# Optimization experiments

Hardware: AMD Instinct MI355X
Metric: run time of the kernel (lower is better)

The kernel has to match this reference:

```python
import jax, jax.numpy as jnp
import numpy as np

RES = 128            # occupancy grid resolution per axis
HIDDEN = 128         # MLP width
PE_POS = 10          # positional-encoding freqs for xyz
PE_DIR = 4           # positional-encoding freqs for viewdirs
S_MAX = 192          # max marching steps per ray
STEP = 0.027         # render_step_size (~aabb diagonal / S_MAX)
ERT = 1e-4           # early_stop_eps (transmittance threshold)
AABB_MIN = -1.5
AABB_MAX = 1.5
WHITE_BKGD = 1.0     # white_bkgd=True


def _posenc(x, L):
    # x: [..., 3] -> [..., 3 + 6L]
    freqs = 2.0 ** jnp.arange(L, dtype=x.dtype)
    xb = x[..., None, :] * freqs[:, None]                 # [..., L, 3]
    enc = jnp.concatenate([jnp.sin(xb), jnp.cos(xb)], axis=-1)  # [..., L, 6]
    return jnp.concatenate([x, enc.reshape(x.shape[:-1] + (-1,))], axis=-1)


def setup_inputs() -> dict:
    key = jax.random.key(0)
    ks = jax.random.split(key, 8)
    B, N = 1, 2048
    # camera origins on a sphere of radius 2.5 outside the aabb, rays aimed near the center
    o = jax.random.normal(ks[0], (B, N, 3), dtype=jnp.float32)
    o = o / jnp.linalg.norm(o, axis=-1, keepdims=True) * 2.5
    target = jax.random.normal(ks[1], (B, N, 3), dtype=jnp.float32) * 0.3
    d = target - o
    d = d / jnp.linalg.norm(d, axis=-1, keepdims=True)
    occ_grid = jax.random.bernoulli(ks[2], 0.3, (RES, RES, RES))
    din_pos = 3 + 6 * PE_POS   # 63
    din_dir = 3 + 6 * PE_DIR   # 27
    sc = lambda n: 1.0 / np.sqrt(n)
    W0 = jax.random.normal(ks[3], (din_pos, HIDDEN), dtype=jnp.float32) * sc(din_pos)
    W1 = jax.random.normal(ks[4], (HIDDEN, HIDDEN), dtype=jnp.float32) * sc(HIDDEN)
    w_sigma = jax.random.normal(ks[5], (HIDDEN, 1), dtype=jnp.float32) * sc(HIDDEN)
    W2 = jax.random.normal(ks[6], (HIDDEN + din_dir, HIDDEN), dtype=jnp.float32) * sc(HIDDEN)
    w_rgb = jax.random.normal(ks[7], (HIDDEN, 3), dtype=jnp.float32) * sc(HIDDEN)
    return {"rays_o": o, "viewdirs": d, "occ_grid": occ_grid,
            "W0": W0, "W1": W1, "w_sigma": w_sigma, "W2": W2, "w_rgb": w_rgb}


def reference(rays_o, viewdirs, occ_grid, W0, W1, w_sigma, W2, w_rgb):
    B, N, _ = rays_o.shape
    o = rays_o.reshape(-1, 3)          # [R, 3]
    d = viewdirs.reshape(-1, 3)        # [R, 3]
    R = o.shape[0]
    # ray / aabb intersection
    inv_d = 1.0 / jnp.where(jnp.abs(d) < 1e-9, 1e-9, d)
    t0 = (AABB_MIN - o) * inv_d
    t1 = (AABB_MAX - o) * inv_d
    t_near = jnp.maximum(jnp.max(jnp.minimum(t0, t1), axis=-1), 0.0)  # [R]
    t_far = jnp.min(jnp.maximum(t0, t1), axis=-1)                     # [R]
    # fixed-step marching (padded to S_MAX, masked) == nerfacc sampling with occ grid
    i = jnp.arange(S_MAX, dtype=rays_o.dtype)
    t_start = t_near[:, None] + STEP * i[None, :]   # [R, S]
    t_end = t_start + STEP
    t_mid = t_start + 0.5 * STEP
    inside = (t_mid < t_far[:, None]) & ((t_far > t_near)[:, None])
    pts = o[:, None, :] + d[:, None, :] * t_mid[..., None]  # [R, S, 3]
    # occupancy lookup (skip empty cells)
    gidx = jnp.clip(((pts - AABB_MIN) / (AABB_MAX - AABB_MIN) * RES).astype(jnp.int32), 0, RES - 1)
    occ = occ_grid[gidx[..., 0], gidx[..., 1], gidx[..., 2]]  # [R, S] bool
    mask = inside & occ
    # NeRF MLP (rgb_alpha_fn): sigma from pos, rgb from pos feature + viewdir
    pe_p = _posenc(pts.reshape(-1, 3), PE_POS)                               # [RS, 63]
    pe_d = _posenc(jnp.broadcast_to(d[:, None, :], pts.shape).reshape(-1, 3), PE_DIR)  # [RS, 27]
    h = jax.nn.relu(pe_p @ W0)
    h = jax.nn.relu(h @ W1)
    sigma = (h @ w_sigma).reshape(R, S_MAX)
    h2 = jax.nn.relu(jnp.concatenate([h, pe_d], axis=-1) @ W2)
    rgb = jax.nn.sigmoid(h2 @ w_rgb).reshape(R, S_MAX, 3)
    # alpha compositing (nerfacc.rendering) with early termination
    delta = t_end - t_start
    alpha = (1.0 - jnp.exp(-jax.nn.relu(sigma) * delta)) * mask.astype(sigma.dtype)
    trans = jnp.cumprod(1.0 - alpha + 1e-10, axis=-1)
    T = jnp.concatenate([jnp.ones((R, 1), alpha.dtype), trans[:, :-1]], axis=-1)  # exclusive
    T = T * (T > ERT).astype(T.dtype)  # early ray termination
    w = T * alpha                      # [R, S]
    rgb_map = jnp.einsum('rs,rsc->rc', w, rgb)
    opacity = jnp.sum(w, axis=-1, keepdims=True)
    depth = jnp.sum(w * t_mid, axis=-1, keepdims=True)
    rgb_map = rgb_map + (1.0 - opacity) * WHITE_BKGD
    return (rgb_map.reshape(B, N, 3), depth.reshape(B, N, 1), opacity.reshape(B, N, 1))
```

## Files before the change

### kernel.cpp

```cpp
#include <hip/hip_runtime.h>
#include <stdint.h>

#define NRAYS 2048
#define SMAX  192
#define RESG  128
#define STEPF 0.027f
#define ERTF  1e-4f

typedef __attribute__((ext_vector_type(8)))  short bf16x8;
typedef __attribute__((ext_vector_type(16))) float f32x16;

__device__ __forceinline__ uint32_t f2b(float x) {
    uint32_t u = __builtin_bit_cast(uint32_t, x);
    return (u + 0x7fffu + ((u >> 16) & 1u)) >> 16;
}
__device__ __forceinline__ uint32_t bpack(float lo, float hi) {
    return f2b(lo) | (f2b(hi) << 16);
}

__device__ __forceinline__ void ray_aabb(float ox, float oy, float oz,
                                         float dx, float dy, float dz,
                                         float& tn, float& tf) {
    float ix = 1.0f / ((fabsf(dx) < 1e-9f) ? 1e-9f : dx);
    float iy = 1.0f / ((fabsf(dy) < 1e-9f) ? 1e-9f : dy);
    float iz = 1.0f / ((fabsf(dz) < 1e-9f) ? 1e-9f : dz);
    float t0x = (-1.5f - ox) * ix, t1x = (1.5f - ox) * ix;
    float t0y = (-1.5f - oy) * iy, t1y = (1.5f - oy) * iy;
    float t0z = (-1.5f - oz) * iz, t1z = (1.5f - oz) * iz;
    float tnx = fminf(t0x, t1x), tfx = fmaxf(t0x, t1x);
    float tny = fminf(t0y, t1y), tfy = fmaxf(t0y, t1y);
    float tnz = fminf(t0z, t1z), tfz = fmaxf(t0z, t1z);
    tn = fmaxf(fmaxf(fmaxf(tnx, tny), tnz), 0.0f);
    tf = fminf(fminf(tfx, tfy), tfz);
}

__global__ __launch_bounds__(512) void k_fused(
        const float* __restrict__ ro, const float* __restrict__ rd,
        const int* __restrict__ occ,
        const float* __restrict__ W0, const float* __restrict__ W1,
        const float* __restrict__ wsig, const float* __restrict__ W2,
        const float* __restrict__ wrgb, float* __restrict__ out) {
    __shared__ __align__(16) short actA[128 * 128];
    __shared__ __align__(16) short bufB[128 * 256];
    __shared__ float4 rgbaL[8 * SMAX];
    __shared__ unsigned short sList[8 * SMAX];
    __shared__ float  sPD[8][28];
    __shared__ float  sRD[8][8];
    __shared__ float  sV[128];
    __shared__ float  sR[384];
    __shared__ int    sCnt[8];

    const int tid  = threadIdx.x;
    const int wave = tid >> 6;
    const int lane = tid & 63;
    const int oc   = wave & 3;
    const int sc   = wave >> 2;
    const int lo5  = lane & 31;
    const int hi5  = lane >> 5;

    if (tid < 128) sV[tid] = wsig[tid];
    if (tid >= 128 && tid < 512) sR[tid - 128] = wrgb[tid - 128];

    bf16x8 wf[22];
    {
        const int outc = oc * 32 + lo5;
        #pragma unroll
        for (int g = 0; g < 22; ++g) {
            const float* W; int kbase, Klim;
            if (g < 4)       { W = W0; kbase = g * 16;        Klim = 63;  }
            else if (g < 12) { W = W1; kbase = (g - 4) * 16;  Klim = 128; }
            else             { W = W2; kbase = (g - 12) * 16; Klim = 155; }
            uint32_t d[4];
            #pragma unroll
            for (int h = 0; h < 4; ++h) {
                int k0 = kbase + (hi5 << 3) + h * 2;
                float lo = (k0     < Klim) ? W[(size_t)k0 * 128 + outc]       : 0.0f;
                float hi = (k0 + 1 < Klim) ? W[(size_t)(k0 + 1) * 128 + outc] : 0.0f;
                d[h] = bpack(lo, hi);
            }
            uint4 v = make_uint4(d[0], d[1], d[2], d[3]);
            wf[g] = __builtin_bit_cast(bf16x8, v);
        }
    }

    const int r = blockIdx.x * 8 + wave;
    const float ox = ro[r*3+0], oy = ro[r*3+1], oz = ro[r*3+2];
    const float dx = rd[r*3+0], dy = rd[r*3+1], dz = rd[r*3+2];
    float tn, tf;
    ray_aabb(ox, oy, oz, dx, dy, dz, tn, tf);
    unsigned long long msk[3];
    int myCnt = 0;
    #pragma unroll
    for (int c = 0; c < 3; ++c) {
        int s = c * 64 + lane;
        float t_mid = (tn + STEPF * (float)s) + 0.5f * STEPF;
        bool inside = (t_mid < tf) && (tf > tn);
        bool act = false;
        if (inside) {
            float px = ox + dx * t_mid;
            float py = oy + dy * t_mid;
            float pz = oz + dz * t_mid;
            int gx = min(max((int)((px + 1.5f) / 3.0f * 128.0f), 0), RESG - 1);
            int gy = min(max((int)((py + 1.5f) / 3.0f * 128.0f), 0), RESG - 1);
            int gz = min(max((int)((pz + 1.5f) / 3.0f * 128.0f), 0), RESG - 1);
            act = occ[(gx * RESG + gy) * RESG + gz] != 0;
        }
        unsigned long long mb = __ballot(act);
        msk[c] = mb;
        myCnt += __popcll(mb);
    }
    if (lane == 0) {
        sCnt[wave] = myCnt;
        sRD[wave][0] = ox; sRD[wave][1] = oy; sRD[wave][2] = oz;
        sRD[wave][3] = dx; sRD[wave][4] = dy; sRD[wave][5] = dz;
        sRD[wave][6] = tn;
    }
    if (lane < 28) {
        float val = 0.0f;
        if (lane < 3) val = (lane == 0) ? dx : ((lane == 1) ? dy : dz);
        else if (lane < 27) {
            int cc = lane - 3, l = cc / 6, jj = cc - 6 * l;
            int a3 = (jj >= 3) ? jj - 3 : jj;
            float comp = (a3 == 0) ? dx : ((a3 == 1) ? dy : dz);
            float arg = comp * (float)(1 << l);
            val = (jj < 3) ? __sinf(arg) : __cosf(arg);
        }
        sPD[wave][lane] = val;
    }
    __syncthreads();

    int myBase = 0, total = 0;
    #pragma unroll
    for (int i = 0; i < 8; ++i) {
        int ci = sCnt[i];
        if (i < wave) myBase += ci;
        total += ci;
    }
    {
        int run = myBase;
        #pragma unroll
        for (int c = 0; c < 3; ++c) {
            unsigned long long mb = msk[c];
            if ((mb >> lane) & 1ull) {
                int within = __popcll(mb & ((1ull << lane) - 1ull));
                sList[run + within] = (unsigned short)((wave << 8) | (c * 64 + lane));
            }
            run += __popcll(mb);
        }
    }
    __syncthreads();

    const int ntiles = (total + 127) >> 7;
    const int mrow   = sc * 64 + lo5;
    const int rswz   = (mrow & 15) << 4;

    for (int t = 0; t < ntiles; ++t) {
        const int base = t << 7;
        __syncthreads();

        {
            int m = tid >> 2, p = tid & 3;
            int gi = base + m;
            float px = 0.f, py = 0.f, pz = 0.f;
            int we = 0;
            if (gi < total) {
                int e = sList[gi];
                we = e >> 8;
                int s = e & 255;
                float tnw = sRD[we][6];
                float t_mid = (tnw + STEPF * (float)s) + 0.5f * STEPF;
                px = sRD[we][0] + sRD[we][3] * t_mid;
                py = sRD[we][1] + sRD[we][4] * t_mid;
                pz = sRD[we][2] + sRD[we][5] * t_mid;
            }
            int swz = (m & 15) << 4;
            #pragma unroll
            for (int half = 0; half < 2; ++half) {
                uint32_t dw[4];
                #pragma unroll
                for (int jp = 0; jp < 4; ++jp) {
                    float v[2];
                    #pragma unroll
                    for (int q = 0; q < 2; ++q) {
                        int c = p * 16 + half * 8 + jp * 2 + q;
                        float val;
                        if (c < 3)        val = (c == 0) ? px : ((c == 1) ? py : pz);
                        else if (c >= 63) val = 0.0f;
                        else {
                            int cc = c - 3, l = cc / 6, jj = cc - 6 * l;
                            int a3 = (jj >= 3) ? jj - 3 : jj;
                            float comp = (a3 == 0) ? px : ((a3 == 1) ? py : pz);
                            float arg = comp * (float)(1 << l);
                            val = (jj < 3) ? __sinf(arg) : __cosf(arg);
                        }
                        v[q] = val;
                    }
                    dw[jp] = bpack(v[0], v[1]);
                }
                *(uint4*)((char*)actA + m * 256 + ((p * 32 + half * 16) ^ swz)) = make_uint4(dw[0], dw[1], dw[2], dw[3]);
            }
            {
                uint32_t dw[4];
                #pragma unroll
                for (int jp = 0; jp < 4; ++jp) {
                    float v[2];
                    #pragma unroll
                    for (int q = 0; q < 2; ++q) {
                        int c = p * 8 + jp * 2 + q;
                        v[q] = (c < 28) ? sPD[we][c] : 0.0f;
                    }
                    dw[jp] = bpack(v[0], v[1]);
                }
                *(uint4*)((char*)bufB + m * 512 + ((256 + p * 16) ^ swz)) = make_uint4(dw[0], dw[1], dw[2], dw[3]);
            }
        }
        __syncthreads();

        {
            f32x16 a0 = {}, a1 = {};
            #pragma unroll
            for (int kb = 0; kb < 4; ++kb) {
                int cb = (kb * 32 + (hi5 << 4)) ^ rswz;
                bf16x8 b0 = *(const bf16x8*)((const char*)actA + mrow * 256 + cb);
                bf16x8 b1 = *(const bf16x8*)((const char*)actA + (mrow + 32) * 256 + cb);
                a0 = __builtin_amdgcn_mfma_f32_32x32x16_bf16(wf[kb], b0, a0, 0, 0, 0);
                a1 = __builtin_amdgcn_mfma_f32_32x32x16_bf16(wf[kb], b1, a1, 0, 0, 0);
            }
            #pragma unroll
            for (int g = 0; g < 4; ++g) {
                int outb = (oc * 32 + g * 8 + (hi5 << 2)) * 2;
                *(uint2*)((char*)bufB + mrow * 512 + (outb ^ rswz)) =
                    make_uint2(bpack(fmaxf(a0[g*4+0],0.f), fmaxf(a0[g*4+1],0.f)),
                               bpack(fmaxf(a0[g*4+2],0.f), fmaxf(a0[g*4+3],0.f)));
                *(uint2*)((char*)bufB + (mrow + 32) * 512 + (outb ^ rswz)) =
                    make_uint2(bpack(fmaxf(a1[g*4+0],0.f), fmaxf(a1[g*4+1],0.f)),
                               bpack(fmaxf(a1[g*4+2],0.f), fmaxf(a1[g*4+3],0.f)));
            }
        }
        __syncthreads();

        {
            f32x16 a0 = {}, a1 = {};
            #pragma unroll
            for (int kb = 0; kb < 8; ++kb) {
                int cb = (kb * 32 + (hi5 << 4)) ^ rswz;
                bf16x8 b0 = *(const bf16x8*)((const char*)bufB + mrow * 512 + cb);
                bf16x8 b1 = *(const bf16x8*)((const char*)bufB + (mrow + 32) * 512 + cb);
                a0 = __builtin_amdgcn_mfma_f32_32x32x16_bf16(wf[4 + kb], b0, a0, 0, 0, 0);
                a1 = __builtin_amdgcn_mfma_f32_32x32x16_bf16(wf[4 + kb], b1, a1, 0, 0, 0);
            }
            #pragma unroll
            for (int g = 0; g < 4; ++g) {
                int outb = (oc * 32 + g * 8 + (hi5 << 2)) * 2;
                *(uint2*)((char*)actA + mrow * 256 + (outb ^ rswz)) =
                    make_uint2(bpack(fmaxf(a0[g*4+0],0.f), fmaxf(a0[g*4+1],0.f)),
                               bpack(fmaxf(a0[g*4+2],0.f), fmaxf(a0[g*4+3],0.f)));
                *(uint2*)((char*)actA + (mrow + 32) * 256 + (outb ^ rswz)) =
                    make_uint2(bpack(fmaxf(a1[g*4+0],0.f), fmaxf(a1[g*4+1],0.f)),
                               bpack(fmaxf(a1[g*4+2],0.f), fmaxf(a1[g*4+3],0.f)));
            }
        }
        __syncthreads();

        {
            f32x16 a0 = {}, a1 = {};
            #pragma unroll
            for (int kb = 0; kb < 8; ++kb) {
                int cb = (kb * 32 + (hi5 << 4)) ^ rswz;
                bf16x8 b0 = *(const bf16x8*)((const char*)actA + mrow * 256 + cb);
                bf16x8 b1 = *(const bf16x8*)((const char*)actA + (mrow + 32) * 256 + cb);
                a0 = __builtin_amdgcn_mfma_f32_32x32x16_bf16(wf[12 + kb], b0, a0, 0, 0, 0);
                a1 = __builtin_amdgcn_mfma_f32_32x32x16_bf16(wf[12 + kb], b1, a1, 0, 0, 0);
            }
            #pragma unroll
            for (int kb = 8; kb < 10; ++kb) {
                int cb = (kb * 32 + (hi5 << 4)) ^ rswz;
                bf16x8 b0 = *(const bf16x8*)((const char*)bufB + mrow * 512 + cb);
                bf16x8 b1 = *(const bf16x8*)((const char*)bufB + (mrow + 32) * 512 + cb);
                a0 = __builtin_amdgcn_mfma_f32_32x32x16_bf16(wf[12 + kb], b0, a0, 0, 0, 0);
                a1 = __builtin_amdgcn_mfma_f32_32x32x16_bf16(wf[12 + kb], b1, a1, 0, 0, 0);
            }
            #pragma unroll
            for (int g = 0; g < 4; ++g) {
                int outb = (oc * 32 + g * 8 + (hi5 << 2)) * 2;
                *(uint2*)((char*)bufB + mrow * 512 + (outb ^ rswz)) =
                    make_uint2(bpack(fmaxf(a0[g*4+0],0.f), fmaxf(a0[g*4+1],0.f)),
                               bpack(fmaxf(a0[g*4+2],0.f), fmaxf(a0[g*4+3],0.f)));
                *(uint2*)((char*)bufB + (mrow + 32) * 512 + (outb ^ rswz)) =
                    make_uint2(bpack(fmaxf(a1[g*4+0],0.f), fmaxf(a1[g*4+1],0.f)),
                               bpack(fmaxf(a1[g*4+2],0.f), fmaxf(a1[g*4+3],0.f)));
            }
        }
        __syncthreads();

        {
            int m = tid >> 2, p = tid & 3;
            int gi = base + m;
            int swz = (m & 15) << 4;
            float sp = 0.f, r0 = 0.f, r1 = 0.f, r2 = 0.f;
            #pragma unroll
            for (int hh = 0; hh < 4; ++hh) {
                uint4 q = *(const uint4*)((const char*)actA + m * 256 + ((p * 64 + hh * 16) ^ swz));
                uint32_t w[4] = {q.x, q.y, q.z, q.w};
                #pragma unroll
                for (int e = 0; e < 4; ++e) {
                    int j = p * 32 + hh * 8 + e * 2;
                    float a0 = __builtin_bit_cast(float, w[e] << 16);
                    float a1 = __builtin_bit_cast(float, w[e] & 0xffff0000u);
                    sp = fmaf(a0, sV[j], sp);
                    sp = fmaf(a1, sV[j + 1], sp);
                }
            }
            #pragma unroll
            for (int hh = 0; hh < 4; ++hh) {
                uint4 q = *(const uint4*)((const char*)bufB + m * 512 + ((p * 64 + hh * 16) ^ swz));
                uint32_t w[4] = {q.x, q.y, q.z, q.w};
                #pragma unroll
                for (int e = 0; e < 4; ++e) {
                    int j = p * 32 + hh * 8 + e * 2;
                    float a0 = __builtin_bit_cast(float, w[e] << 16);
                    float a1 = __builtin_bit_cast(float, w[e] & 0xffff0000u);
                    r0 = fmaf(a0, sR[j*3+0], r0); r1 = fmaf(a0, sR[j*3+1], r1); r2 = fmaf(a0, sR[j*3+2], r2);
                    r0 = fmaf(a1, sR[(j+1)*3+0], r0); r1 = fmaf(a1, sR[(j+1)*3+1], r1); r2 = fmaf(a1, sR[(j+1)*3+2], r2);
                }
            }
            #pragma unroll
            for (int off = 1; off < 4; off <<= 1) {
                sp += __shfl_xor(sp, off);
                r0 += __shfl_xor(r0, off);
                r1 += __shfl_xor(r1, off);
                r2 += __shfl_xor(r2, off);
            }
            if (p == 0 && gi < total) {
                float alpha = 1.0f - __expf(-fmaxf(sp, 0.0f) * STEPF);
                float c0 = 1.0f / (1.0f + __expf(-r0));
                float c1 = 1.0f / (1.0f + __expf(-r1));
                float c2 = 1.0f / (1.0f + __expf(-r2));
                rgbaL[gi] = make_float4(c0, c1, c2, alpha);
            }
        }
    }
    __syncthreads();

    {
        float T_run = 1.0f;
        float cr = 0.f, cg = 0.f, cb = 0.f, opa = 0.f, dep = 0.f;
        for (int j = 0; j < myCnt; j += 64) {
            int idx = j + lane;
            float4 f = make_float4(0.f, 0.f, 0.f, 0.f);
            float tmid = 0.f;
            if (idx < myCnt) {
                f = rgbaL[myBase + idx];
                int s = sList[myBase + idx] & 255;
                tmid = (tn + STEPF * (float)s) + 0.5f * STEPF;
            }
            float p = (1.0f - f.w) + 1e-10f;
            #pragma unroll
            for (int o = 1; o < 64; o <<= 1) {
                float v = __shfl_up(p, o);
                if (lane >= o) p *= v;
            }
            float pprev = __shfl_up(p, 1);
            float Texc = (lane == 0) ? T_run : T_run * pprev;
            Texc = (Texc > ERTF) ? Texc : 0.0f;
            float w = Texc * f.w;
            cr += w * f.x; cg += w * f.y; cb += w * f.z;
            opa += w; dep += w * tmid;
            T_run *= __shfl(p, 63);
            if (T_run <= ERTF) break;
        }
        #pragma unroll
        for (int o = 32; o; o >>= 1) {
            cr  += __shfl_xor(cr, o);
            cg  += __shfl_xor(cg, o);
            cb  += __shfl_xor(cb, o);
            opa += __shfl_xor(opa, o);
            dep += __shfl_xor(dep, o);
        }
        if (lane == 0) {
            out[r * 3 + 0] = cr + (1.0f - opa);
            out[r * 3 + 1] = cg + (1.0f - opa);
            out[r * 3 + 2] = cb + (1.0f - opa);
            out[NRAYS * 3 + r] = dep;
            out[NRAYS * 4 + r] = opa;
        }
    }
}

extern "C" void kernel_launch(void* const* d_in, const int* in_sizes, int n_in,
                              void* d_out, int out_size, void* d_ws, size_t ws_size,
                              hipStream_t stream) {
    const float* ro   = (const float*)d_in[0];
    const float* rd   = (const float*)d_in[1];
    const int*   occ  = (const int*)d_in[2];
    const float* W0   = (const float*)d_in[3];
    const float* W1   = (const float*)d_in[4];
    const float* wsig = (const float*)d_in[5];
    const float* W2   = (const float*)d_in[6];
    const float* wrgb = (const float*)d_in[7];
    float* out = (float*)d_out;

    k_fused<<<NRAYS / 8, 512, 0, stream>>>(ro, rd, occ, W0, W1, wsig, W2, wrgb, out);
}
```

Before: 115.6 us.

## Halve rays per block to four and use 64-row MLP tiles

Each 512-thread block now handles 4 rays instead of 8, doubling the grid to 512 blocks. The MLP tile shrinks from 128 to 64 sample rows, so each wave runs one MFMA chain instead of two. Encoding and head work is split across 8 threads per row. Shared memory drops to about half, and launch bounds request 4 blocks per CU, to raise occupancy and spread work over more CUs on a small problem. The cost is that half the waves sit idle during ray setup and compositing, per-block weight fragment loads double in total, and per-tile sync overhead becomes relatively larger.

After: 189.7 us. 1.64x slower.

```diff
diff --git a/kernel.cpp b/kernel.cpp
--- a/kernel.cpp
+++ b/kernel.cpp
@@ -34,21 +34,21 @@
     tf = fminf(fminf(tfx, tfy), tfz);
 }
 
-__global__ __launch_bounds__(512) void k_fused(
+__global__ __launch_bounds__(512, 4) void k_fused(
         const float* __restrict__ ro, const float* __restrict__ rd,
         const int* __restrict__ occ,
         const float* __restrict__ W0, const float* __restrict__ W1,
         const float* __restrict__ wsig, const float* __restrict__ W2,
         const float* __restrict__ wrgb, float* __restrict__ out) {
-    __shared__ __align__(16) short actA[128 * 128];
-    __shared__ __align__(16) short bufB[128 * 256];
-    __shared__ float4 rgbaL[8 * SMAX];
-    __shared__ unsigned short sList[8 * SMAX];
-    __shared__ float  sPD[8][28];
-    __shared__ float  sRD[8][8];
+    __shared__ __align__(16) short actA[64 * 128];
+    __shared__ __align__(16) short bufB[64 * 256];
+    __shared__ float4 rgbaL[4 * SMAX];
+    __shared__ unsigned short sList[4 * SMAX];
+    __shared__ float  sPD[4][28];
+    __shared__ float  sRD[4][8];
     __shared__ float  sV[128];
     __shared__ float  sR[384];
-    __shared__ int    sCnt[8];
+    __shared__ int    sCnt[4];
 
     const int tid  = threadIdx.x;
     const int wave = tid >> 6;
@@ -83,60 +83,63 @@
         }
     }
 
-    const int r = blockIdx.x * 8 + wave;
-    const float ox = ro[r*3+0], oy = ro[r*3+1], oz = ro[r*3+2];
-    const float dx = rd[r*3+0], dy = rd[r*3+1], dz = rd[r*3+2];
-    float tn, tf;
-    ray_aabb(ox, oy, oz, dx, dy, dz, tn, tf);
     unsigned long long msk[3];
     int myCnt = 0;
-    #pragma unroll
-    for (int c = 0; c < 3; ++c) {
-        int s = c * 64 + lane;
-        float t_mid = (tn + STEPF * (float)s) + 0.5f * STEPF;
-        bool inside = (t_mid < tf) && (tf > tn);
-        bool act = false;
-        if (inside) {
-            float px = ox + dx * t_mid;
-            float py = oy + dy * t_mid;
-            float pz = oz + dz * t_mid;
-            int gx = min(max((int)((px + 1.5f) / 3.0f * 128.0f), 0), RESG - 1);
-            int gy = min(max((int)((py + 1.5f) / 3.0f * 128.0f), 0), RESG - 1);
-            int gz = min(max((int)((pz + 1.5f) / 3.0f * 128.0f), 0), RESG - 1);
-            act = occ[(gx * RESG + gy) * RESG + gz] != 0;
-        }
-        unsigned long long mb = __ballot(act);
-        msk[c] = mb;
-        myCnt += __popcll(mb);
-    }
-    if (lane == 0) {
-        sCnt[wave] = myCnt;
-        sRD[wave][0] = ox; sRD[wave][1] = oy; sRD[wave][2] = oz;
-        sRD[wave][3] = dx; sRD[wave][4] = dy; sRD[wave][5] = dz;
-        sRD[wave][6] = tn;
-    }
-    if (lane < 28) {
-        float val = 0.0f;
-        if (lane < 3) val = (lane == 0) ? dx : ((lane == 1) ? dy : dz);
-        else if (lane < 27) {
-            int cc = lane - 3, l = cc / 6, jj = cc - 6 * l;
-            int a3 = (jj >= 3) ? jj - 3 : jj;
-            float comp = (a3 == 0) ? dx : ((a3 == 1) ? dy : dz);
-            float arg = comp * (float)(1 << l);
-            val = (jj < 3) ? __sinf(arg) : __cosf(arg);
-        }
-        sPD[wave][lane] = val;
+    float tn = 0.f;
+    const int r = blockIdx.x * 4 + wave;
+    if (wave < 4) {
+        const float ox = ro[r*3+0], oy = ro[r*3+1], oz = ro[r*3+2];
+        const float dx = rd[r*3+0], dy = rd[r*3+1], dz = rd[r*3+2];
+        float tf;
+        ray_aabb(ox, oy, oz, dx, dy, dz, tn, tf);
+        #pragma unroll
+        for (int c = 0; c < 3; ++c) {
+            int s = c * 64 + lane;
+            float t_mid = (tn + STEPF * (float)s) + 0.5f * STEPF;
+            bool inside = (t_mid < tf) && (tf > tn);
+            bool act = false;
+            if (inside) {
+                float px = ox + dx * t_mid;
+                float py = oy + dy * t_mid;
+                float pz = oz + dz * t_mid;
+                int gx = min(max((int)((px + 1.5f) / 3.0f * 128.0f), 0), RESG - 1);
+                int gy = min(max((int)((py + 1.5f) / 3.0f * 128.0f), 0), RESG - 1);
+                int gz = min(max((int)((pz + 1.5f) / 3.0f * 128.0f), 0), RESG - 1);
+                act = occ[(gx * RESG + gy) * RESG + gz] != 0;
+            }
+            unsigned long long mb = __ballot(act);
+            msk[c] = mb;
+            myCnt += __popcll(mb);
+        }
+        if (lane == 0) {
+            sCnt[wave] = myCnt;
+            sRD[wave][0] = ox; sRD[wave][1] = oy; sRD[wave][2] = oz;
+            sRD[wave][3] = dx; sRD[wave][4] = dy; sRD[wave][5] = dz;
+            sRD[wave][6] = tn;
+        }
+        if (lane < 28) {
+            float val = 0.0f;
+            if (lane < 3) val = (lane == 0) ? dx : ((lane == 1) ? dy : dz);
+            else if (lane < 27) {
+                int cc = lane - 3, l = cc / 6, jj = cc - 6 * l;
+                int a3 = (jj >= 3) ? jj - 3 : jj;
+                float comp = (a3 == 0) ? dx : ((a3 == 1) ? dy : dz);
+                float arg = comp * (float)(1 << l);
+                val = (jj < 3) ? __sinf(arg) : __cosf(arg);
+            }
+            sPD[wave][lane] = val;
+        }
     }
     __syncthreads();
 
     int myBase = 0, total = 0;
     #pragma unroll
-    for (int i = 0; i < 8; ++i) {
+    for (int i = 0; i < 4; ++i) {
         int ci = sCnt[i];
         if (i < wave) myBase += ci;
         total += ci;
     }
-    {
+    if (wave < 4) {
         int run = myBase;
         #pragma unroll
         for (int c = 0; c < 3; ++c) {
@@ -150,16 +153,16 @@
     }
     __syncthreads();
 
-    const int ntiles = (total + 127) >> 7;
-    const int mrow   = sc * 64 + lo5;
+    const int ntiles = (total + 63) >> 6;
+    const int mrow   = sc * 32 + lo5;
     const int rswz   = (mrow & 15) << 4;
 
     for (int t = 0; t < ntiles; ++t) {
-        const int base = t << 7;
-        __syncthreads();
-
-        {
-            int m = tid >> 2, p = tid & 3;
+        const int base = t << 6;
+        __syncthreads();
+
+        {
+            int m = tid >> 3, p = tid & 7;
             int gi = base + m;
             float px = 0.f, py = 0.f, pz = 0.f;
             int we = 0;
@@ -174,33 +177,29 @@
                 pz = sRD[we][2] + sRD[we][5] * t_mid;
             }
             int swz = (m & 15) << 4;
-            #pragma unroll
-            for (int half = 0; half < 2; ++half) {
-                uint32_t dw[4];
+            uint32_t dw[4];
+            #pragma unroll
+            for (int jp = 0; jp < 4; ++jp) {
+                float v[2];
                 #pragma unroll
-                for (int jp = 0; jp < 4; ++jp) {
-                    float v[2];
-                    #pragma unroll
-                    for (int q = 0; q < 2; ++q) {
-                        int c = p * 16 + half * 8 + jp * 2 + q;
-                        float val;
-                        if (c < 3)        val = (c == 0) ? px : ((c == 1) ? py : pz);
-                        else if (c >= 63) val = 0.0f;
-                        else {
-                            int cc = c - 3, l = cc / 6, jj = cc - 6 * l;
-                            int a3 = (jj >= 3) ? jj - 3 : jj;
-                            float comp = (a3 == 0) ? px : ((a3 == 1) ? py : pz);
-                            float arg = comp * (float)(1 << l);
-                            val = (jj < 3) ? __sinf(arg) : __cosf(arg);
-                        }
-                        v[q] = val;
+                for (int q = 0; q < 2; ++q) {
+                    int c = p * 8 + jp * 2 + q;
+                    float val;
+                    if (c < 3)        val = (c == 0) ? px : ((c == 1) ? py : pz);
+                    else if (c >= 63) val = 0.0f;
+                    else {
+                        int cc = c - 3, l = cc / 6, jj = cc - 6 * l;
+                        int a3 = (jj >= 3) ? jj - 3 : jj;
+                        float comp = (a3 == 0) ? px : ((a3 == 1) ? py : pz);
+                        float arg = comp * (float)(1 << l);
+                        val = (jj < 3) ? __sinf(arg) : __cosf(arg);
                     }
-                    dw[jp] = bpack(v[0], v[1]);
+                    v[q] = val;
                 }
-                *(uint4*)((char*)actA + m * 256 + ((p * 32 + half * 16) ^ swz)) = make_uint4(dw[0], dw[1], dw[2], dw[3]);
-            }
-            {
-                uint32_t dw[4];
+                dw[jp] = bpack(v[0], v[1]);
+            }
+            *(uint4*)((char*)actA + m * 256 + ((p * 16) ^ swz)) = make_uint4(dw[0], dw[1], dw[2], dw[3]);
+            if (p < 4) {
                 #pragma unroll
                 for (int jp = 0; jp < 4; ++jp) {
                     float v[2];
@@ -217,94 +216,73 @@
         __syncthreads();
 
         {
-            f32x16 a0 = {}, a1 = {};
+            f32x16 acc = {};
             #pragma unroll
             for (int kb = 0; kb < 4; ++kb) {
-                int cb = (kb * 32 + (hi5 << 4)) ^ rswz;
-                bf16x8 b0 = *(const bf16x8*)((const char*)actA + mrow * 256 + cb);
-                bf16x8 b1 = *(const bf16x8*)((const char*)actA + (mrow + 32) * 256 + cb);
-                a0 = __builtin_amdgcn_mfma_f32_32x32x16_bf16(wf[kb], b0, a0, 0, 0, 0);
-                a1 = __builtin_amdgcn_mfma_f32_32x32x16_bf16(wf[kb], b1, a1, 0, 0, 0);
+                bf16x8 bf = *(const bf16x8*)((const char*)actA + mrow * 256 + ((kb * 32 + (hi5 << 4)) ^ rswz));
+                acc = __builtin_amdgcn_mfma_f32_32x32x16_bf16(wf[kb], bf, acc, 0, 0, 0);
             }
             #pragma unroll
             for (int g = 0; g < 4; ++g) {
                 int outb = (oc * 32 + g * 8 + (hi5 << 2)) * 2;
                 *(uint2*)((char*)bufB + mrow * 512 + (outb ^ rswz)) =
-                    make_uint2(bpack(fmaxf(a0[g*4+0],0.f), fmaxf(a0[g*4+1],0.f)),
-                               bpack(fmaxf(a0[g*4+2],0.f), fmaxf(a0[g*4+3],0.f)));
-                *(uint2*)((char*)bufB + (mrow + 32) * 512 + (outb ^ rswz)) =
-                    make_uint2(bpack(fmaxf(a1[g*4+0],0.f), fmaxf(a1[g*4+1],0.f)),
-                               bpack(fmaxf(a1[g*4+2],0.f), fmaxf(a1[g*4+3],0.f)));
-            }
-        }
-        __syncthreads();
-
-        {
-            f32x16 a0 = {}, a1 = {};
+                    make_uint2(bpack(fmaxf(acc[g*4+0],0.f), fmaxf(acc[g*4+1],0.f)),
+                               bpack(fmaxf(acc[g*4+2],0.f), fmaxf(acc[g*4+3],0.f)));
+            }
+        }
+        __syncthreads();
+
+        {
+            f32x16 acc = {};
             #pragma unroll
             for (int kb = 0; kb < 8; ++kb) {
-                int cb = (kb * 32 + (hi5 << 4)) ^ rswz;
-                bf16x8 b0 = *(const bf16x8*)((const char*)bufB + mrow * 512 + cb);
-                bf16x8 b1 = *(const bf16x8*)((const char*)bufB + (mrow + 32) * 512 + cb);
-                a0 = __builtin_amdgcn_mfma_f32_32x32x16_bf16(wf[4 + kb], b0, a0, 0, 0, 0);
-                a1 = __builtin_amdgcn_mfma_f32_32x32x16_bf16(wf[4 + kb], b1, a1, 0, 0, 0);
+                bf16x8 bf = *(const bf16x8*)((const char*)bufB + mrow * 512 + ((kb * 32 + (hi5 << 4)) ^ rswz));
+                acc = __builtin_amdgcn_mfma_f32_32x32x16_bf16(wf[4 + kb], bf, acc, 0, 0, 0);
             }
             #pragma unroll
             for (int g = 0; g < 4; ++g) {
                 int outb = (oc * 32 + g * 8 + (hi5 << 2)) * 2;
                 *(uint2*)((char*)actA + mrow * 256 + (outb ^ rswz)) =
-                    make_uint2(bpack(fmaxf(a0[g*4+0],0.f), fmaxf(a0[g*4+1],0.f)),
-                               bpack(fmaxf(a0[g*4+2],0.f), fmaxf(a0[g*4+3],0.f)));
-                *(uint2*)((char*)actA + (mrow + 32) * 256 + (outb ^ rswz)) =
-                    make_uint2(bpack(fmaxf(a1[g*4+0],0.f), fmaxf(a1[g*4+1],0.f)),
-                               bpack(fmaxf(a1[g*4+2],0.f), fmaxf(a1[g*4+3],0.f)));
-            }
-        }
-        __syncthreads();
-
-        {
-            f32x16 a0 = {}, a1 = {};
+                    make_uint2(bpack(fmaxf(acc[g*4+0],0.f), fmaxf(acc[g*4+1],0.f)),
+                               bpack(fmaxf(acc[g*4+2],0.f), fmaxf(acc[g*4+3],0.f)));
+            }
+        }
+        __syncthreads();
+
+        {
+            f32x16 acc = {};
             #pragma unroll
             for (int kb = 0; kb < 8; ++kb) {
-                int cb = (kb * 32 + (hi5 << 4)) ^ rswz;
-                bf16x8 b0 = *(const bf16x8*)((const char*)actA + mrow * 256 + cb);
-                bf16x8 b1 = *(const bf16x8*)((const char*)actA + (mrow + 32) * 256 + cb);
-                a0 = __builtin_amdgcn_mfma_f32_32x32x16_bf16(wf[12 + kb], b0, a0, 0, 0, 0);
-                a1 = __builtin_amdgcn_mfma_f32_32x32x16_bf16(wf[12 + kb], b1, a1, 0, 0, 0);
+                bf16x8 bf = *(const bf16x8*)((const char*)actA + mrow * 256 + ((kb * 32 + (hi5 << 4)) ^ rswz));
+                acc = __builtin_amdgcn_mfma_f32_32x32x16_bf16(wf[12 + kb], bf, acc, 0, 0, 0);
             }
             #pragma unroll
             for (int kb = 8; kb < 10; ++kb) {
-                int cb = (kb * 32 + (hi5 << 4)) ^ rswz;
-                bf16x8 b0 = *(const bf16x8*)((const char*)bufB + mrow * 512 + cb);
-                bf16x8 b1 = *(const bf16x8*)((const char*)bufB + (mrow + 32) * 512 + cb);
-                a0 = __builtin_amdgcn_mfma_f32_32x32x16_bf16(wf[12 + kb], b0, a0, 0, 0, 0);
-                a1 = __builtin_amdgcn_mfma_f32_32x32x16_bf16(wf[12 + kb], b1, a1, 0, 0, 0);
+                bf16x8 bf = *(const bf16x8*)((const char*)bufB + mrow * 512 + ((kb * 32 + (hi5 << 4)) ^ rswz));
+                acc = __builtin_amdgcn_mfma_f32_32x32x16_bf16(wf[12 + kb], bf, acc, 0, 0, 0);
             }
             #pragma unroll
             for (int g = 0; g < 4; ++g) {
                 int outb = (oc * 32 + g * 8 + (hi5 << 2)) * 2;
                 *(uint2*)((char*)bufB + mrow * 512 + (outb ^ rswz)) =
-                    make_uint2(bpack(fmaxf(a0[g*4+0],0.f), fmaxf(a0[g*4+1],0.f)),
-                               bpack(fmaxf(a0[g*4+2],0.f), fmaxf(a0[g*4+3],0.f)));
-                *(uint2*)((char*)bufB + (mrow + 32) * 512 + (outb ^ rswz)) =
-                    make_uint2(bpack(fmaxf(a1[g*4+0],0.f), fmaxf(a1[g*4+1],0.f)),
-                               bpack(fmaxf(a1[g*4+2],0.f), fmaxf(a1[g*4+3],0.f)));
-            }
-        }
-        __syncthreads();
-
-        {
-            int m = tid >> 2, p = tid & 3;
+                    make_uint2(bpack(fmaxf(acc[g*4+0],0.f), fmaxf(acc[g*4+1],0.f)),
+                               bpack(fmaxf(acc[g*4+2],0.f), fmaxf(acc[g*4+3],0.f)));
+            }
+        }
+        __syncthreads();
+
+        {
+            int m = tid >> 3, p = tid & 7;
             int gi = base + m;
             int swz = (m & 15) << 4;
             float sp = 0.f, r0 = 0.f, r1 = 0.f, r2 = 0.f;
             #pragma unroll
-            for (int hh = 0; hh < 4; ++hh) {
-                uint4 q = *(const uint4*)((const char*)actA + m * 256 + ((p * 64 + hh * 16) ^ swz));
+            for (int hh = 0; hh < 2; ++hh) {
+                uint4 q = *(const uint4*)((const char*)actA + m * 256 + ((p * 32 + hh * 16) ^ swz));
                 uint32_t w[4] = {q.x, q.y, q.z, q.w};
                 #pragma unroll
                 for (int e = 0; e < 4; ++e) {
-                    int j = p * 32 + hh * 8 + e * 2;
+                    int j = p * 16 + hh * 8 + e * 2;
                     float a0 = __builtin_bit_cast(float, w[e] << 16);
                     float a1 = __builtin_bit_cast(float, w[e] & 0xffff0000u);
                     sp = fmaf(a0, sV[j], sp);
@@ -312,12 +290,12 @@
                 }
             }
             #pragma unroll
-            for (int hh = 0; hh < 4; ++hh) {
-                uint4 q = *(const uint4*)((const char*)bufB + m * 512 + ((p * 64 + hh * 16) ^ swz));
+            for (int hh = 0; hh < 2; ++hh) {
+                uint4 q = *(const uint4*)((const char*)bufB + m * 512 + ((p * 32 + hh * 16) ^ swz));
                 uint32_t w[4] = {q.x, q.y, q.z, q.w};
                 #pragma unroll
                 for (int e = 0; e < 4; ++e) {
-                    int j = p * 32 + hh * 8 + e * 2;
+                    int j = p * 16 + hh * 8 + e * 2;
                     float a0 = __builtin_bit_cast(float, w[e] << 16);
                     float a1 = __builtin_bit_cast(float, w[e] & 0xffff0000u);
                     r0 = fmaf(a0, sR[j*3+0], r0); r1 = fmaf(a0, sR[j*3+1], r1); r2 = fmaf(a0, sR[j*3+2], r2);
@@ -325,7 +303,7 @@
                 }
             }
             #pragma unroll
-            for (int off = 1; off < 4; off <<= 1) {
+            for (int off = 1; off < 8; off <<= 1) {
                 sp += __shfl_xor(sp, off);
                 r0 += __shfl_xor(r0, off);
                 r1 += __shfl_xor(r1, off);
@@ -342,7 +320,7 @@
     }
     __syncthreads();
 
-    {
+    if (wave < 4) {
         float T_run = 1.0f;
         float cr = 0.f, cg = 0.f, cb = 0.f, opa = 0.f, dep = 0.f;
         for (int j = 0; j < myCnt; j += 64) {
@@ -400,5 +378,5 @@
     const float* wrgb = (const float*)d_in[7];
     float* out = (float*)d_out;
 
-    k_fused<<<NRAYS / 8, 512, 0, stream>>>(ro, rd, occ, W0, W1, wsig, W2, wrgb, out);
-}
+    k_fused<<<NRAYS / 4, 512, 0, stream>>>(ro, rd, occ, W0, W1, wsig, W2, wrgb, out);
+}
```
